# Kernel optimization log

Measured on AMD Instinct MI355X. Metric: run time of the kernel, lower is better.

## Reference

```python
import jax, jax.numpy as jnp
import numpy as np

BT, N = 4, 2048
FIN, FOUT = 512, 128          # GGE in/out; FOUT == PPI output (GAGA constraint)
PIN, POUT = 256, 128          # PPIGE in/out
HEAD = 4
K = POUT // HEAD              # per-head dim = 32
NEG_SLOPE = 0.2
MASK_VAL = -1e30


def setup_inputs() -> dict:
    key = jax.random.key(0)
    ks = jax.random.split(key, 24)
    s = 0.05
    inp = {}
    inp["a"] = jax.random.normal(ks[0], (BT, FIN), jnp.float32)
    inp["bio_a"] = jax.random.normal(ks[1], (BT, N, PIN), jnp.float32)
    inp["A"] = jax.random.randint(ks[2], (BT, N, N), 0, 2, jnp.int32)
    inp["b"] = jax.random.normal(ks[3], (BT, FIN), jnp.float32)
    inp["bio_b"] = jax.random.normal(ks[4], (BT, N, PIN), jnp.float32)
    inp["B"] = jax.random.randint(ks[5], (BT, N, N), 0, 2, jnp.int32)
    # PPIGE_GAT params (shared across both graph branches)
    inp["initW"] = jax.random.normal(ks[6], (POUT, PIN), jnp.float32) * s
    inp["initb"] = jnp.zeros((POUT,), jnp.float32)
    inp["projW"] = jax.random.normal(ks[7], (POUT, POUT), jnp.float32) * s  # no bias
    inp["attw"] = jax.random.normal(ks[8], (HEAD, 2 * K), jnp.float32) * s  # per-head [2k]->1
    inp["attb"] = jnp.zeros((HEAD,), jnp.float32)
    # GGE params
    inp["ggeW1"] = jax.random.normal(ks[9], (128, FIN), jnp.float32) * s
    inp["ggeb1"] = jnp.zeros((128,), jnp.float32)
    inp["ggeW2"] = jax.random.normal(ks[10], (FOUT, 128), jnp.float32) * s
    inp["ggeb2"] = jnp.zeros((FOUT,), jnp.float32)
    # LED params (hidden = FOUT)
    inp["convW"] = jax.random.normal(ks[11], (2 * FOUT, 2 * FOUT), jnp.float32) * s  # k=1 conv
    inp["convb"] = jnp.zeros((2 * FOUT,), jnp.float32)
    inp["ledW1"] = jax.random.normal(ks[12], (FOUT, 4 * FOUT), jnp.float32) * s
    inp["ledb1"] = jnp.zeros((FOUT,), jnp.float32)
    inp["ledW2"] = jax.random.normal(ks[13], (2, FOUT), jnp.float32) * s
    inp["ledb2"] = jnp.zeros((2,), jnp.float32)
    return inp


def _gat_layer(x, adj_mask, projW, attw, attb):
    # x: [B,N,POUT]; adj_mask: [B,N,N] bool
    Bt, n, _ = x.shape
    xh = (x @ projW.T).reshape(Bt, n, HEAD, K).transpose(0, 2, 1, 3)  # [B,h,N,k]
    # score(i,j) = leaky_relu(w1.x_i + w2.x_j + b)  (equivalent to Linear on concat)
    s1 = jnp.einsum('bhnk,hk->bhn', xh, attw[:, :K])
    s2 = jnp.einsum('bhnk,hk->bhn', xh, attw[:, K:])
    scores = jax.nn.leaky_relu(
        s1[..., :, None] + s2[..., None, :] + attb[None, :, None, None], NEG_SLOPE)
    scores = jnp.where(adj_mask[:, None], scores, MASK_VAL)
    att = jax.nn.softmax(scores, axis=-1)                     # [B,h,N,N]
    out = jax.nn.relu(att @ xh)                               # [B,h,N,k]
    return out.transpose(0, 2, 1, 3).reshape(Bt, n, HEAD * K)


def _ppige(bio, adj, initW, initb, projW, attw, attb):
    x = bio @ initW.T + initb
    return _gat_layer(x, adj > 0, projW, attw, attb) + x      # residual; dropout=eval


def _gge(a, W1, b1, W2, b2):
    h = jax.nn.relu(a @ W1.T + b1)
    return jax.nn.relu(h @ W2.T + b2)


def _gaga(G, h):
    # G: [B,N,D], h: [B,D]
    att = jax.nn.softmax(jnp.einsum('bnd,bd->bn', G, h), axis=-1)
    return jnp.einsum('bnd,bn->bd', G, att)


def _led(ea, eb, convW, convb, W1, b1, W2, b2):
    # pointwise conv over the length-2 stack [ea, eb], then maxpool over length
    cnn = jnp.maximum(ea @ convW.T + convb, eb @ convW.T + convb)  # [B,2D]
    x = jax.nn.relu(jnp.concatenate([cnn, ea - eb], axis=1) @ W1.T + b1)
    return x @ W2.T + b2


def reference(a, bio_a, A, b, bio_b, B,
              initW, initb, projW, attw, attb,
              ggeW1, ggeb1, ggeW2, ggeb2,
              convW, convb, ledW1, ledb1, ledW2, ledb2):
    G_a = _ppige(bio_a, A, initW, initb, projW, attw, attb)
    G_b = _ppige(bio_b, B, initW, initb, projW, attw, attb)
    h_a = _gge(a, ggeW1, ggeb1, ggeW2, ggeb2)
    h_b = _gge(b, ggeW1, ggeb1, ggeW2, ggeb2)
    e_a = jnp.concatenate([h_a, _gaga(G_a, h_a)], axis=-1)
    e_b = jnp.concatenate([h_b, _gaga(G_b, h_b)], axis=-1)
    logits = _led(e_a, e_b, convW, convb, ledW1, ledb1, ledW2, ledb2)
    return jax.nn.log_softmax(logits, axis=-1)
```

## Files before the change

kernel.cpp:

```cpp
#include <hip/hip_runtime.h>
#include <hip/hip_bf16.h>
#include <math.h>

#define NN 2048
#define NEG 0.2f
#define LOG2E 1.44269504f

typedef short bf16x8 __attribute__((ext_vector_type(8)));
typedef float f32x16 __attribute__((ext_vector_type(16)));

__device__ __forceinline__ float dot4(float4 a, float4 b) {
  return a.x * b.x + a.y * b.y + a.z * b.z + a.w * b.w;
}

__device__ __forceinline__ unsigned short bfbits(float f) {
  union { __hip_bfloat16 b; unsigned short u; } c;
  c.b = __float2bfloat16(f);
  return c.u;
}

__global__ __launch_bounds__(256) void k12_fused(const float* __restrict__ bioA,
                                                 const float* __restrict__ bioB,
                                                 const float* __restrict__ initW,
                                                 const float* __restrict__ initb,
                                                 const float* __restrict__ projW,
                                                 const float* __restrict__ attw,
                                                 float* __restrict__ xout,
                                                 unsigned short* __restrict__ xhT2,
                                                 float* __restrict__ s1,
                                                 float* __restrict__ s2) {
  __shared__ float As[32][36];
  __shared__ float Ws[32][132];
  __shared__ float xT[128][36];
  const int t = threadIdx.x;
  const int m0 = blockIdx.x * 32;
  const float* A = (m0 < 8192) ? bioA : bioB;
  const int arow0 = (m0 < 8192) ? m0 : (m0 - 8192);
  const int og = t & 31, ig = t >> 5;

  float acc[4][4] = {};
  for (int kt = 0; kt < 256; kt += 32) {
    __syncthreads();
    {
      const int r = t >> 3, kq = t & 7;
      const float4 v = *(const float4*)&A[(arow0 + r) * 256 + kt + kq * 4];
      As[kq * 4 + 0][r] = v.x; As[kq * 4 + 1][r] = v.y;
      As[kq * 4 + 2][r] = v.z; As[kq * 4 + 3][r] = v.w;
    }
#pragma unroll
    for (int u = 0; u < 4; ++u) {
      const int f = u * 256 + t;
      const int o = f >> 3, kq = f & 7;
      const float4 v = *(const float4*)&initW[o * 256 + kt + kq * 4];
      Ws[kq * 4 + 0][o] = v.x; Ws[kq * 4 + 1][o] = v.y;
      Ws[kq * 4 + 2][o] = v.z; Ws[kq * 4 + 3][o] = v.w;
    }
    __syncthreads();
#pragma unroll
    for (int kk = 0; kk < 32; ++kk) {
      const float4 a4 = *(const float4*)&As[kk][ig * 4];
      const float4 w4 = *(const float4*)&Ws[kk][og * 4];
      const float av[4] = {a4.x, a4.y, a4.z, a4.w};
      const float wv[4] = {w4.x, w4.y, w4.z, w4.w};
#pragma unroll
      for (int ii = 0; ii < 4; ++ii)
#pragma unroll
        for (int jj = 0; jj < 4; ++jj) acc[ii][jj] += av[ii] * wv[jj];
    }
  }
  {
    const float4 b4 = *(const float4*)&initb[og * 4];
    const float bj[4] = {b4.x, b4.y, b4.z, b4.w};
#pragma unroll
    for (int ii = 0; ii < 4; ++ii) {
      const int row = m0 + ig * 4 + ii;
      float4 o4;
      o4.x = acc[ii][0] + bj[0]; o4.y = acc[ii][1] + bj[1];
      o4.z = acc[ii][2] + bj[2]; o4.w = acc[ii][3] + bj[3];
      *(float4*)&xout[row * 128 + og * 4] = o4;
    }
#pragma unroll
    for (int jj = 0; jj < 4; ++jj) {
      float4 v;
      v.x = acc[0][jj] + bj[jj]; v.y = acc[1][jj] + bj[jj];
      v.z = acc[2][jj] + bj[jj]; v.w = acc[3][jj] + bj[jj];
      *(float4*)&xT[og * 4 + jj][ig * 4] = v;
    }
  }
  __syncthreads();

  float acc2[4][4] = {};
  for (int kt = 0; kt < 128; kt += 32) {
    __syncthreads();
#pragma unroll
    for (int u = 0; u < 4; ++u) {
      const int f = u * 256 + t;
      const int o = f >> 3, kq = f & 7;
      const float4 v = *(const float4*)&projW[o * 128 + kt + kq * 4];
      Ws[kq * 4 + 0][o] = v.x; Ws[kq * 4 + 1][o] = v.y;
      Ws[kq * 4 + 2][o] = v.z; Ws[kq * 4 + 3][o] = v.w;
    }
    __syncthreads();
#pragma unroll
    for (int kk = 0; kk < 32; ++kk) {
      const float4 a4 = *(const float4*)&xT[kt + kk][ig * 4];
      const float4 w4 = *(const float4*)&Ws[kk][og * 4];
      const float av[4] = {a4.x, a4.y, a4.z, a4.w};
      const float wv[4] = {w4.x, w4.y, w4.z, w4.w};
#pragma unroll
      for (int ii = 0; ii < 4; ++ii)
#pragma unroll
        for (int jj = 0; jj < 4; ++jj) acc2[ii][jj] += av[ii] * wv[jj];
    }
  }
  const int h = og >> 3;
  const int k4i = (og & 7) * 4;
  const int g = m0 >> 13;
  const int bb = (m0 >> 11) & 3;
  const int gb = g * 4 + bb;
  const int n0 = (m0 & 2047) + ig * 4;
  const float4 w1 = *(const float4*)&attw[h * 64 + k4i];
  const float4 w2 = *(const float4*)&attw[h * 64 + 32 + k4i];
  float p1[4], p2[4];
#pragma unroll
  for (int ii = 0; ii < 4; ++ii) {
    float4 v;
    v.x = acc2[ii][0]; v.y = acc2[ii][1]; v.z = acc2[ii][2]; v.w = acc2[ii][3];
    p1[ii] = dot4(v, w1);
    p2[ii] = dot4(v, w2);
  }
  {
    const int mtile = n0 >> 4, jslot = (n0 >> 3) & 1, j8 = n0 & 7;
    const int base2 = ((((gb * 4 + h) * 128 + mtile) * 2 + jslot) * 32) * 8 + j8;
#pragma unroll
    for (int jj = 0; jj < 4; ++jj) {
      const int kin = k4i + jj;
      ushort4 u;
      u.x = bfbits(acc2[0][jj]); u.y = bfbits(acc2[1][jj]);
      u.z = bfbits(acc2[2][jj]); u.w = bfbits(acc2[3][jj]);
      *(ushort4*)&xhT2[base2 + kin * 8] = u;
    }
  }
#pragma unroll
  for (int s = 1; s < 8; s <<= 1) {
#pragma unroll
    for (int ii = 0; ii < 4; ++ii) {
      p1[ii] += __shfl_xor(p1[ii], s);
      p2[ii] += __shfl_xor(p2[ii], s);
    }
  }
  if ((og & 7) == 0) {
#pragma unroll
    for (int ii = 0; ii < 4; ++ii) {
      s1[(gb * 4 + h) * NN + n0 + ii] = p1[ii];
      s2[(gb * 4 + h) * NN + n0 + ii] = p2[ii];
    }
  }
}

#define K3_PROLOGUE                                                           \
  {                                                                           \
    const float* s2g = s2w + gb * 4 * NN;                                     \
    _Pragma("unroll")                                                         \
    for (int u = 0; u < 4; ++u) {                                             \
      const int idx = u * 2048 + t * 4;                                       \
      float4 v = *(const float4*)&s2g[idx];                                   \
      v.x *= LOG2E; v.y *= LOG2E; v.z *= LOG2E; v.w *= LOG2E;                 \
      *(float4*)&s2L[idx] = v;                                                \
    }                                                                         \
  }                                                                           \
  _Pragma("unroll")                                                           \
  for (int r4 = 0; r4 < 4; ++r4) {                                            \
    const int r = wave * 4 + r4;                                              \
    const int* arow = adj + r * NN;                                           \
    int av[32];                                                               \
    _Pragma("unroll")                                                         \
    for (int w = 0; w < 32; ++w) av[w] = __builtin_nontemporal_load(&arow[w * 64 + lane]); \
    _Pragma("unroll")                                                         \
    for (int w = 0; w < 32; ++w) {                                            \
      const unsigned long long mm = __ballot(av[w] > 0);                      \
      if (lane < 2) adjL[r * 66 + 2 * w + lane] = (unsigned int)(mm >> (32 * lane)); \
    }                                                                         \
  }

#define K3_SCORE_BODY(MM)                                                     \
    const int j0 = jlo + 16 * (MM) + jslot * 8;                               \
    const unsigned int wbits = adjL[i * 66 + ((jlo + 16 * (MM)) >> 5)];       \
    const unsigned int bits8 = wbits >> ((((MM) & 1) * 16) + jslot * 8);      \
    const float4 s2a = *(const float4*)&s2L[h * 2048 + j0];                   \
    const float4 s2b = *(const float4*)&s2L[h * 2048 + j0 + 4];               \
    const float sv[8] = {s2a.x, s2a.y, s2a.z, s2a.w,                          \
                         s2b.x, s2b.y, s2b.z, s2b.w};                         \
    union { bf16x8 v; unsigned short u[8]; } af;                              \
    float dsum = 0.f;                                                         \
    _Pragma("unroll")                                                         \
    for (int e = 0; e < 8; ++e) {                                             \
      float s = sc1v + sv[e];                                                 \
      s = fmaxf(s, NEG * s);                                                  \
      float pe = __builtin_amdgcn_exp2f(s);                                   \
      pe = ((bits8 >> e) & 1u) ? pe : 0.f;                                    \
      af.u[e] = bfbits(pe);                                                   \
      dsum += pe;                                                             \
    }                                                                         \
    den += dsum;

__global__ __launch_bounds__(512) void k3_attn(const unsigned short* __restrict__ xhT2,
                                               const float* __restrict__ s1w,
                                               const float* __restrict__ s2w,
                                               const int* __restrict__ adjA,
                                               const int* __restrict__ adjB,
                                               const float* __restrict__ attb,
                                               const float* __restrict__ x,
                                               float* __restrict__ G) {
  __shared__ __align__(16) unsigned char smem3[42240];
  unsigned int* adjL = (unsigned int*)smem3;
  float* s2L = (float*)(smem3 + 8448);
  float* denR = (float*)(smem3 + 41216);
  float* accR = (float*)smem3;

  const int t = threadIdx.x;
  const int wave = t >> 6, lane = t & 63;
  const int p = (int)blockIdx.x;
  const int blk = (p & 7) * 64 + (p >> 3);
  const int g = blk >> 8, b = (blk >> 6) & 3;
  const int i0 = (blk & 63) * 32;
  const int gb = g * 4 + b;
  const int* adj = (g ? adjB : adjA) + (b * NN + i0) * NN;
  K3_PROLOGUE
  __syncthreads();

  const int h = wave & 3;
  const int jhalf = wave >> 2;
  const int jlo = jhalf * 1024;
  const int i = lane & 31;
  const int jslot = lane >> 5;
  const float sc1v = (s1w[(gb * 4 + h) * NN + i0 + i] + attb[h]) * LOG2E;
  const unsigned short* bbase = xhT2 + (gb * 4 + h) * 65536 + jhalf * 32768 + lane * 8;
  f32x16 acc = {0.f, 0.f, 0.f, 0.f, 0.f, 0.f, 0.f, 0.f,
                0.f, 0.f, 0.f, 0.f, 0.f, 0.f, 0.f, 0.f};
  float den = 0.f;

#define K3_CSTEP(RB, MM)                                                      \
  {                                                                           \
    K3_SCORE_BODY(MM)                                                         \
    acc = __builtin_amdgcn_mfma_f32_32x32x16_bf16(af.v, RB, acc, 0, 0, 0);    \
  }

  bf16x8 fa0 = *(const bf16x8*)&bbase[0 * 512];
  bf16x8 fa1 = *(const bf16x8*)&bbase[1 * 512];
  bf16x8 fa2 = *(const bf16x8*)&bbase[2 * 512];
  bf16x8 fa3 = *(const bf16x8*)&bbase[3 * 512];
  bf16x8 fb0 = *(const bf16x8*)&bbase[4 * 512];
  bf16x8 fb1 = *(const bf16x8*)&bbase[5 * 512];
  bf16x8 fb2 = *(const bf16x8*)&bbase[6 * 512];
  bf16x8 fb3 = *(const bf16x8*)&bbase[7 * 512];
  bf16x8 fc0 = *(const bf16x8*)&bbase[8 * 512];
  bf16x8 fc1 = *(const bf16x8*)&bbase[9 * 512];
  bf16x8 fc2 = *(const bf16x8*)&bbase[10 * 512];
  bf16x8 fc3 = *(const bf16x8*)&bbase[11 * 512];
  bf16x8 fd0 = *(const bf16x8*)&bbase[12 * 512];
  bf16x8 fd1 = *(const bf16x8*)&bbase[13 * 512];
  bf16x8 fd2 = *(const bf16x8*)&bbase[14 * 512];
  bf16x8 fd3 = *(const bf16x8*)&bbase[15 * 512];
  __builtin_amdgcn_sched_barrier(0);
  for (int mb = 0; mb < 64; mb += 16) {
    K3_CSTEP(fa0, mb + 0)
    K3_CSTEP(fa1, mb + 1)
    K3_CSTEP(fa2, mb + 2)
    K3_CSTEP(fa3, mb + 3)
    __builtin_amdgcn_sched_barrier(0);
    if (mb < 48) {
      fa0 = *(const bf16x8*)&bbase[(mb + 16) * 512];
      fa1 = *(const bf16x8*)&bbase[(mb + 17) * 512];
      fa2 = *(const bf16x8*)&bbase[(mb + 18) * 512];
      fa3 = *(const bf16x8*)&bbase[(mb + 19) * 512];
    }
    __builtin_amdgcn_sched_barrier(0);
    K3_CSTEP(fb0, mb + 4)
    K3_CSTEP(fb1, mb + 5)
    K3_CSTEP(fb2, mb + 6)
    K3_CSTEP(fb3, mb + 7)
    __builtin_amdgcn_sched_barrier(0);
    if (mb < 48) {
      fb0 = *(const bf16x8*)&bbase[(mb + 20) * 512];
      fb1 = *(const bf16x8*)&bbase[(mb + 21) * 512];
      fb2 = *(const bf16x8*)&bbase[(mb + 22) * 512];
      fb3 = *(const bf16x8*)&bbase[(mb + 23) * 512];
    }
    __builtin_amdgcn_sched_barrier(0);
    K3_CSTEP(fc0, mb + 8)
    K3_CSTEP(fc1, mb + 9)
    K3_CSTEP(fc2, mb + 10)
    K3_CSTEP(fc3, mb + 11)
    __builtin_amdgcn_sched_barrier(0);
    if (mb < 48) {
      fc0 = *(const bf16x8*)&bbase[(mb + 24) * 512];
      fc1 = *(const bf16x8*)&bbase[(mb + 25) * 512];
      fc2 = *(const bf16x8*)&bbase[(mb + 26) * 512];
      fc3 = *(const bf16x8*)&bbase[(mb + 27) * 512];
    }
    __builtin_amdgcn_sched_barrier(0);
    K3_CSTEP(fd0, mb + 12)
    K3_CSTEP(fd1, mb + 13)
    K3_CSTEP(fd2, mb + 14)
    K3_CSTEP(fd3, mb + 15)
    __builtin_amdgcn_sched_barrier(0);
    if (mb < 48) {
      fd0 = *(const bf16x8*)&bbase[(mb + 28) * 512];
      fd1 = *(const bf16x8*)&bbase[(mb + 29) * 512];
      fd2 = *(const bf16x8*)&bbase[(mb + 30) * 512];
      fd3 = *(const bf16x8*)&bbase[(mb + 31) * 512];
    }
    __builtin_amdgcn_sched_barrier(0);
  }
#undef K3_CSTEP

  den += __shfl_xor(den, 32);
  if (lane < 32) denR[(h * 2 + jhalf) * 32 + lane] = den;
  __syncthreads();
  if (jhalf == 1) {
#pragma unroll
    for (int r = 0; r < 16; ++r) accR[(h * 16 + r) * 65 + lane] = acc[r];
  }
  __syncthreads();
  if (jhalf == 0) {
#pragma unroll
    for (int r = 0; r < 16; ++r) {
      const int row = (r & 3) + 8 * (r >> 2) + 4 * jslot;
      const float dinv = 1.f / (denR[(h * 2 + 0) * 32 + row] + denR[(h * 2 + 1) * 32 + row]);
      const int off = (gb * NN + i0 + row) * 128 + h * 32 + i;
      const float av2 = acc[r] + accR[(h * 16 + r) * 65 + lane];
      G[off] = fmaxf(av2 * dinv, 0.f) + x[off];
    }
  }
}

__global__ __launch_bounds__(256) void k4h_gge(const float* __restrict__ a_in,
                                               const float* __restrict__ b_in,
                                               const float* __restrict__ ggeW1,
                                               const float* __restrict__ ggeb1,
                                               const float* __restrict__ ggeW2,
                                               const float* __restrict__ ggeb2,
                                               float* __restrict__ hvbuf,
                                               float* __restrict__ e) {
  __shared__ float inL[512];
  __shared__ float h1L[128];
  const int t = threadIdx.x;
  const int wave = t >> 6, lane = t & 63;
  const int g = blockIdx.x >> 2, b = blockIdx.x & 3;
  const int gb2 = g * 4 + b;
  const float* inp = (g ? b_in : a_in) + b * 512;
  if (t < 128) *(float4*)&inL[t * 4] = *(const float4*)&inp[t * 4];
  __syncthreads();
  for (int p = 0; p < 16; ++p) {
    const int o0 = p * 8 + wave * 2;
    const float* w0 = &ggeW1[o0 * 512 + lane * 8];
    const float* w1 = &ggeW1[(o0 + 1) * 512 + lane * 8];
    const float4 i0v = *(const float4*)&inL[lane * 8];
    const float4 i1v = *(const float4*)&inL[lane * 8 + 4];
    float s0 = dot4(*(const float4*)&w0[0], i0v) + dot4(*(const float4*)&w0[4], i1v);
    float s1v = dot4(*(const float4*)&w1[0], i0v) + dot4(*(const float4*)&w1[4], i1v);
#pragma unroll
    for (int s = 1; s < 64; s <<= 1) { s0 += __shfl_xor(s0, s); s1v += __shfl_xor(s1v, s); }
    if (lane == 0) {
      h1L[o0] = fmaxf(s0 + ggeb1[o0], 0.f);
      h1L[o0 + 1] = fmaxf(s1v + ggeb1[o0 + 1], 0.f);
    }
  }
  __syncthreads();
  for (int p = 0; p < 16; ++p) {
    const int o0 = p * 8 + wave * 2;
    const float2 w0 = *(const float2*)&ggeW2[o0 * 128 + lane * 2];
    const float2 w1 = *(const float2*)&ggeW2[(o0 + 1) * 128 + lane * 2];
    const float2 hvv = *(const float2*)&h1L[lane * 2];
    float s0 = w0.x * hvv.x + w0.y * hvv.y;
    float s1v = w1.x * hvv.x + w1.y * hvv.y;
#pragma unroll
    for (int s = 1; s < 64; s <<= 1) { s0 += __shfl_xor(s0, s); s1v += __shfl_xor(s1v, s); }
    if (lane == 0) {
      const float v0 = fmaxf(s0 + ggeb2[o0], 0.f);
      const float v1 = fmaxf(s1v + ggeb2[o0 + 1], 0.f);
      hvbuf[gb2 * 128 + o0] = v0;
      hvbuf[gb2 * 128 + o0 + 1] = v1;
      e[gb2 * 256 + o0] = v0;
      e[gb2 * 256 + o0 + 1] = v1;
    }
  }
}

__global__ __launch_bounds__(256) void k4a_gaga(const float* __restrict__ G,
                                                const float* __restrict__ hv,
                                                float* __restrict__ wsumC,
                                                float* __restrict__ mzC) {
  __shared__ float lgL[128];
  __shared__ float pL[128];
  __shared__ float red[256];
  __shared__ float red2[2][128];
  const int t = threadIdx.x;
  const int wave = t >> 6, lane = t & 63;
  const int gb = blockIdx.x >> 4, chunk = blockIdx.x & 15;
  const float2 hvv = *(const float2*)&hv[gb * 128 + lane * 2];
  const float* Gb = G + (gb * NN + chunk * 128) * 128;
  const int nbase = wave * 32;
  for (int q = 0; q < 32; ++q) {
    const int n = nbase + q;
    const float2 gv = *(const float2*)&Gb[n * 128 + lane * 2];
    float part = gv.x * hvv.x + gv.y * hvv.y;
#pragma unroll
    for (int s = 1; s < 64; s <<= 1) part += __shfl_xor(part, s);
    if (lane == 0) lgL[n] = part;
  }
  __syncthreads();
  red[t] = (t < 128) ? lgL[t] : -1e30f;
  __syncthreads();
#pragma unroll
  for (int s = 128; s > 0; s >>= 1) {
    if (t < s) red[t] = fmaxf(red[t], red[t + s]);
    __syncthreads();
  }
  const float mc = red[0];
  __syncthreads();
  if (t < 128) {
    const float pv = __expf(lgL[t] - mc);
    pL[t] = pv;
    red[t] = pv;
  } else red[t] = 0.f;
  __syncthreads();
#pragma unroll
  for (int s = 128; s > 0; s >>= 1) {
    if (t < s) red[t] += red[t + s];
    __syncthreads();
  }
  const float zc = red[0];
  __syncthreads();
  const int d = t & 127, half = t >> 7;
  const float* Gh = Gb + (half * 64) * 128;
  float acc = 0.f;
  for (int q = 0; q < 64; ++q) acc += pL[half * 64 + q] * Gh[q * 128 + d];
  red2[half][d] = acc;
  __syncthreads();
  if (t < 128) wsumC[(gb * 16 + chunk) * 128 + t] = red2[0][t] + red2[1][t];
  if (t == 0) {
    mzC[(gb * 16 + chunk) * 2 + 0] = mc;
    mzC[(gb * 16 + chunk) * 2 + 1] = zc;
  }
}

__global__ __launch_bounds__(256) void k5_led(const float* __restrict__ e,
                                              const float* __restrict__ wsumC,
                                              const float* __restrict__ mzC,
                                              const float* __restrict__ convW,
                                              const float* __restrict__ convb,
                                              const float* __restrict__ ledW1,
                                              const float* __restrict__ ledb1,
                                              const float* __restrict__ ledW2,
                                              const float* __restrict__ ledb2,
                                              float* __restrict__ out) {
  __shared__ float eaL[256], ebL[256], uL[512], xL[128], lgL[2];
  const int t = threadIdx.x;
  const int wave = t >> 6, lane = t & 63;
  const int bt = blockIdx.x;
  const int gba = bt, gbb = 4 + bt;
  if (t < 128) {
    eaL[t] = e[gba * 256 + t];
    ebL[t] = e[gbb * 256 + t];
    float ma = -1e30f, mb2 = -1e30f;
#pragma unroll
    for (int c = 0; c < 16; ++c) {
      ma = fmaxf(ma, mzC[(gba * 16 + c) * 2]);
      mb2 = fmaxf(mb2, mzC[(gbb * 16 + c) * 2]);
    }
    float Za = 0.f, Zb = 0.f, sa = 0.f, sb = 0.f;
#pragma unroll
    for (int c = 0; c < 16; ++c) {
      const float wa = __expf(mzC[(gba * 16 + c) * 2] - ma);
      const float wb = __expf(mzC[(gbb * 16 + c) * 2] - mb2);
      Za += mzC[(gba * 16 + c) * 2 + 1] * wa;
      Zb += mzC[(gbb * 16 + c) * 2 + 1] * wb;
      sa += wsumC[(gba * 16 + c) * 128 + t] * wa;
      sb += wsumC[(gbb * 16 + c) * 128 + t] * wb;
    }
    eaL[128 + t] = sa / Za;
    ebL[128 + t] = sb / Zb;
  }
  __syncthreads();
  uL[256 + t] = eaL[t] - ebL[t];
  const float4 ea4 = *(const float4*)&eaL[lane * 4];
  const float4 eb4 = *(const float4*)&ebL[lane * 4];
  for (int p = 0; p < 32; ++p) {
    const int o0 = p * 8 + wave * 2;
    const float4 w0 = *(const float4*)&convW[o0 * 256 + lane * 4];
    const float4 w1 = *(const float4*)&convW[(o0 + 1) * 256 + lane * 4];
    float sa0 = dot4(w0, ea4), sb0 = dot4(w0, eb4);
    float sa1 = dot4(w1, ea4), sb1 = dot4(w1, eb4);
#pragma unroll
    for (int s = 1; s < 64; s <<= 1) {
      sa0 += __shfl_xor(sa0, s); sb0 += __shfl_xor(sb0, s);
      sa1 += __shfl_xor(sa1, s); sb1 += __shfl_xor(sb1, s);
    }
    if (lane == 0) {
      const float c0 = convb[o0], c1 = convb[o0 + 1];
      uL[o0] = fmaxf(sa0 + c0, sb0 + c0);
      uL[o0 + 1] = fmaxf(sa1 + c1, sb1 + c1);
    }
  }
  __syncthreads();
  for (int p = 0; p < 16; ++p) {
    const int o0 = p * 8 + wave * 2;
    const float* w0 = &ledW1[o0 * 512 + lane * 8];
    const float* w1 = &ledW1[(o0 + 1) * 512 + lane * 8];
    const float4 u0 = *(const float4*)&uL[lane * 8];
    const float4 u1 = *(const float4*)&uL[lane * 8 + 4];
    float s0 = dot4(*(const float4*)&w0[0], u0) + dot4(*(const float4*)&w0[4], u1);
    float s1v = dot4(*(const float4*)&w1[0], u0) + dot4(*(const float4*)&w1[4], u1);
#pragma unroll
    for (int s = 1; s < 64; s <<= 1) { s0 += __shfl_xor(s0, s); s1v += __shfl_xor(s1v, s); }
    if (lane == 0) {
      xL[o0] = fmaxf(s0 + ledb1[o0], 0.f);
      xL[o0 + 1] = fmaxf(s1v + ledb1[o0 + 1], 0.f);
    }
  }
  __syncthreads();
  if (wave < 2) {
    const float2 w = *(const float2*)&ledW2[wave * 128 + lane * 2];
    const float2 xv = *(const float2*)&xL[lane * 2];
    float s0 = w.x * xv.x + w.y * xv.y;
#pragma unroll
    for (int s = 1; s < 64; s <<= 1) s0 += __shfl_xor(s0, s);
    if (lane == 0) lgL[wave] = s0 + ledb2[wave];
  }
  __syncthreads();
  if (t == 0) {
    const float l0 = lgL[0], l1 = lgL[1];
    const float m = fmaxf(l0, l1);
    const float za = __expf(l0 - m) + __expf(l1 - m);
    const float lz = __logf(za);
    out[bt * 2 + 0] = l0 - m - lz;
    out[bt * 2 + 1] = l1 - m - lz;
  }
}

extern "C" void kernel_launch(void* const* d_in, const int* in_sizes, int n_in,
                              void* d_out, int out_size, void* d_ws, size_t ws_size,
                              hipStream_t stream) {
  (void)in_sizes; (void)n_in; (void)out_size; (void)ws_size;
  const float* a     = (const float*)d_in[0];
  const float* bioA  = (const float*)d_in[1];
  const int*   A     = (const int*)d_in[2];
  const float* b     = (const float*)d_in[3];
  const float* bioB  = (const float*)d_in[4];
  const int*   B     = (const int*)d_in[5];
  const float* initW = (const float*)d_in[6];
  const float* initb = (const float*)d_in[7];
  const float* projW = (const float*)d_in[8];
  const float* attw  = (const float*)d_in[9];
  const float* attb  = (const float*)d_in[10];
  const float* ggeW1 = (const float*)d_in[11];
  const float* ggeb1 = (const float*)d_in[12];
  const float* ggeW2 = (const float*)d_in[13];
  const float* ggeb2 = (const float*)d_in[14];
  const float* convW = (const float*)d_in[15];
  const float* convb = (const float*)d_in[16];
  const float* ledW1 = (const float*)d_in[17];
  const float* ledb1 = (const float*)d_in[18];
  const float* ledW2 = (const float*)d_in[19];
  const float* ledb2 = (const float*)d_in[20];

  float* ws = (float*)d_ws;
  float*          x     = ws;
  unsigned short* xhT2  = (unsigned short*)(ws + 2097152);
  float*          s1    = ws + 3145728;
  float*          s2    = ws + 3211264;
  float*          G     = ws + 3276800;
  float*          mzC   = ws + 5373952;
  float*          wsumC = ws + 5390336;
  float*          hv    = ws + 5406736;
  float*          e     = ws + 5407760;
  float* out = (float*)d_out;

  k12_fused<<<512, 256, 0, stream>>>(bioA, bioB, initW, initb, projW, attw,
                                     x, xhT2, s1, s2);
  k3_attn<<<512, 512, 0, stream>>>(xhT2, s1, s2, A, B, attb, x, G);
  k4h_gge<<<8, 256, 0, stream>>>(a, b, ggeW1, ggeb1, ggeW2, ggeb2, hv, e);
  k4a_gaga<<<128, 256, 0, stream>>>(G, hv, wsumC, mzC);
  k5_led<<<4, 256, 0, stream>>>(e, wsumC, mzC, convW, convb, ledW1, ledb1,
                                ledW2, ledb2, out);
}
```

Measured before the change: 182.4 us.

## Fuse GGE into projection kernel and GAGA partial softmax into attention epilogue

The GGE MLP now runs on eight extra blocks appended to the projection kernel launch. The GAGA logits, per-chunk softmax max and sum, and the weighted sum over G are computed in the attention kernel epilogue, one chunk per 32-row tile. This removes two kernel launches and the separate re-read of G by the old GAGA kernel. In exchange the final LED kernel must merge 64 chunks per graph instead of 16, and the epilogue re-reads G from global memory just after writing it.

Measured after the change: 165.0 us (median of 2 runs). 1.11x faster.

```diff
diff --git a/kernel.cpp b/kernel.cpp
--- a/kernel.cpp
+++ b/kernel.cpp
@@ -25,14 +25,70 @@
                                                  const float* __restrict__ initb,
                                                  const float* __restrict__ projW,
                                                  const float* __restrict__ attw,
+                                                 const float* __restrict__ a_in,
+                                                 const float* __restrict__ b_in,
+                                                 const float* __restrict__ ggeW1,
+                                                 const float* __restrict__ ggeb1,
+                                                 const float* __restrict__ ggeW2,
+                                                 const float* __restrict__ ggeb2,
                                                  float* __restrict__ xout,
                                                  unsigned short* __restrict__ xhT2,
                                                  float* __restrict__ s1,
-                                                 float* __restrict__ s2) {
+                                                 float* __restrict__ s2,
+                                                 float* __restrict__ hvbuf,
+                                                 float* __restrict__ e) {
   __shared__ float As[32][36];
   __shared__ float Ws[32][132];
   __shared__ float xT[128][36];
   const int t = threadIdx.x;
+  const int wave = t >> 6, lane = t & 63;
+
+  if (blockIdx.x >= 512) {
+    float* inL = (float*)As;
+    float* h1L = ((float*)As) + 512;
+    const int bb2 = (int)blockIdx.x - 512;
+    const int g = bb2 >> 2, b = bb2 & 3;
+    const int gb2 = g * 4 + b;
+    const float* inp = (g ? b_in : a_in) + b * 512;
+    if (t < 128) *(float4*)&inL[t * 4] = *(const float4*)&inp[t * 4];
+    __syncthreads();
+    for (int p = 0; p < 16; ++p) {
+      const int o0 = p * 8 + wave * 2;
+      const float* w0 = &ggeW1[o0 * 512 + lane * 8];
+      const float* w1 = &ggeW1[(o0 + 1) * 512 + lane * 8];
+      const float4 i0v = *(const float4*)&inL[lane * 8];
+      const float4 i1v = *(const float4*)&inL[lane * 8 + 4];
+      float s0 = dot4(*(const float4*)&w0[0], i0v) + dot4(*(const float4*)&w0[4], i1v);
+      float s1v = dot4(*(const float4*)&w1[0], i0v) + dot4(*(const float4*)&w1[4], i1v);
+#pragma unroll
+      for (int s = 1; s < 64; s <<= 1) { s0 += __shfl_xor(s0, s); s1v += __shfl_xor(s1v, s); }
+      if (lane == 0) {
+        h1L[o0] = fmaxf(s0 + ggeb1[o0], 0.f);
+        h1L[o0 + 1] = fmaxf(s1v + ggeb1[o0 + 1], 0.f);
+      }
+    }
+    __syncthreads();
+    for (int p = 0; p < 16; ++p) {
+      const int o0 = p * 8 + wave * 2;
+      const float2 w0 = *(const float2*)&ggeW2[o0 * 128 + lane * 2];
+      const float2 w1 = *(const float2*)&ggeW2[(o0 + 1) * 128 + lane * 2];
+      const float2 hvv = *(const float2*)&h1L[lane * 2];
+      float s0 = w0.x * hvv.x + w0.y * hvv.y;
+      float s1v = w1.x * hvv.x + w1.y * hvv.y;
+#pragma unroll
+      for (int s = 1; s < 64; s <<= 1) { s0 += __shfl_xor(s0, s); s1v += __shfl_xor(s1v, s); }
+      if (lane == 0) {
+        const float v0 = fmaxf(s0 + ggeb2[o0], 0.f);
+        const float v1 = fmaxf(s1v + ggeb2[o0 + 1], 0.f);
+        hvbuf[gb2 * 128 + o0] = v0;
+        hvbuf[gb2 * 128 + o0 + 1] = v1;
+        e[gb2 * 256 + o0] = v0;
+        e[gb2 * 256 + o0 + 1] = v1;
+      }
+    }
+    return;
+  }
+
   const int m0 = blockIdx.x * 32;
   const float* A = (m0 < 8192) ? bioA : bioB;
   const int arow0 = (m0 < 8192) ? m0 : (m0 - 8192);
@@ -211,12 +267,17 @@
                                                const int* __restrict__ adjB,
                                                const float* __restrict__ attb,
                                                const float* __restrict__ x,
-                                               float* __restrict__ G) {
+                                               const float* __restrict__ hv,
+                                               float* __restrict__ G,
+                                               float* __restrict__ wsumC,
+                                               float* __restrict__ mzC) {
   __shared__ __align__(16) unsigned char smem3[42240];
   unsigned int* adjL = (unsigned int*)smem3;
   float* s2L = (float*)(smem3 + 8448);
   float* denR = (float*)(smem3 + 41216);
   float* accR = (float*)smem3;
+  float* lgW = (float*)(smem3 + 16640);
+  float* pL = (float*)(smem3 + 17280);
 
   const int t = threadIdx.x;
   const int wave = t >> 6, lane = t & 63;
@@ -225,6 +286,7 @@
   const int g = blk >> 8, b = (blk >> 6) & 3;
   const int i0 = (blk & 63) * 32;
   const int gb = g * 4 + b;
+  const int cidx = gb * 64 + (blk & 63);
   const int* adj = (g ? adjB : adjA) + (b * NN + i0) * NN;
   K3_PROLOGUE
   __syncthreads();
@@ -323,6 +385,7 @@
     for (int r = 0; r < 16; ++r) accR[(h * 16 + r) * 65 + lane] = acc[r];
   }
   __syncthreads();
+  const float hvv = hv[gb * 128 + h * 32 + i];
   if (jhalf == 0) {
 #pragma unroll
     for (int r = 0; r < 16; ++r) {
@@ -330,119 +393,39 @@
       const float dinv = 1.f / (denR[(h * 2 + 0) * 32 + row] + denR[(h * 2 + 1) * 32 + row]);
       const int off = (gb * NN + i0 + row) * 128 + h * 32 + i;
       const float av2 = acc[r] + accR[(h * 16 + r) * 65 + lane];
-      G[off] = fmaxf(av2 * dinv, 0.f) + x[off];
-    }
-  }
-}
-
-__global__ __launch_bounds__(256) void k4h_gge(const float* __restrict__ a_in,
-                                               const float* __restrict__ b_in,
-                                               const float* __restrict__ ggeW1,
-                                               const float* __restrict__ ggeb1,
-                                               const float* __restrict__ ggeW2,
-                                               const float* __restrict__ ggeb2,
-                                               float* __restrict__ hvbuf,
-                                               float* __restrict__ e) {
-  __shared__ float inL[512];
-  __shared__ float h1L[128];
-  const int t = threadIdx.x;
-  const int wave = t >> 6, lane = t & 63;
-  const int g = blockIdx.x >> 2, b = blockIdx.x & 3;
-  const int gb2 = g * 4 + b;
-  const float* inp = (g ? b_in : a_in) + b * 512;
-  if (t < 128) *(float4*)&inL[t * 4] = *(const float4*)&inp[t * 4];
-  __syncthreads();
-  for (int p = 0; p < 16; ++p) {
-    const int o0 = p * 8 + wave * 2;
-    const float* w0 = &ggeW1[o0 * 512 + lane * 8];
-    const float* w1 = &ggeW1[(o0 + 1) * 512 + lane * 8];
-    const float4 i0v = *(const float4*)&inL[lane * 8];
-    const float4 i1v = *(const float4*)&inL[lane * 8 + 4];
-    float s0 = dot4(*(const float4*)&w0[0], i0v) + dot4(*(const float4*)&w0[4], i1v);
-    float s1v = dot4(*(const float4*)&w1[0], i0v) + dot4(*(const float4*)&w1[4], i1v);
-#pragma unroll
-    for (int s = 1; s < 64; s <<= 1) { s0 += __shfl_xor(s0, s); s1v += __shfl_xor(s1v, s); }
-    if (lane == 0) {
-      h1L[o0] = fmaxf(s0 + ggeb1[o0], 0.f);
-      h1L[o0 + 1] = fmaxf(s1v + ggeb1[o0 + 1], 0.f);
-    }
-  }
-  __syncthreads();
-  for (int p = 0; p < 16; ++p) {
-    const int o0 = p * 8 + wave * 2;
-    const float2 w0 = *(const float2*)&ggeW2[o0 * 128 + lane * 2];
-    const float2 w1 = *(const float2*)&ggeW2[(o0 + 1) * 128 + lane * 2];
-    const float2 hvv = *(const float2*)&h1L[lane * 2];
-    float s0 = w0.x * hvv.x + w0.y * hvv.y;
-    float s1v = w1.x * hvv.x + w1.y * hvv.y;
-#pragma unroll
-    for (int s = 1; s < 64; s <<= 1) { s0 += __shfl_xor(s0, s); s1v += __shfl_xor(s1v, s); }
-    if (lane == 0) {
-      const float v0 = fmaxf(s0 + ggeb2[o0], 0.f);
-      const float v1 = fmaxf(s1v + ggeb2[o0 + 1], 0.f);
-      hvbuf[gb2 * 128 + o0] = v0;
-      hvbuf[gb2 * 128 + o0 + 1] = v1;
-      e[gb2 * 256 + o0] = v0;
-      e[gb2 * 256 + o0 + 1] = v1;
-    }
-  }
-}
-
-__global__ __launch_bounds__(256) void k4a_gaga(const float* __restrict__ G,
-                                                const float* __restrict__ hv,
-                                                float* __restrict__ wsumC,
-                                                float* __restrict__ mzC) {
-  __shared__ float lgL[128];
-  __shared__ float pL[128];
-  __shared__ float red[256];
-  __shared__ float red2[2][128];
-  const int t = threadIdx.x;
-  const int wave = t >> 6, lane = t & 63;
-  const int gb = blockIdx.x >> 4, chunk = blockIdx.x & 15;
-  const float2 hvv = *(const float2*)&hv[gb * 128 + lane * 2];
-  const float* Gb = G + (gb * NN + chunk * 128) * 128;
-  const int nbase = wave * 32;
-  for (int q = 0; q < 32; ++q) {
-    const int n = nbase + q;
-    const float2 gv = *(const float2*)&Gb[n * 128 + lane * 2];
-    float part = gv.x * hvv.x + gv.y * hvv.y;
-#pragma unroll
-    for (int s = 1; s < 64; s <<= 1) part += __shfl_xor(part, s);
-    if (lane == 0) lgL[n] = part;
-  }
-  __syncthreads();
-  red[t] = (t < 128) ? lgL[t] : -1e30f;
-  __syncthreads();
-#pragma unroll
-  for (int s = 128; s > 0; s >>= 1) {
-    if (t < s) red[t] = fmaxf(red[t], red[t + s]);
-    __syncthreads();
-  }
-  const float mc = red[0];
-  __syncthreads();
-  if (t < 128) {
-    const float pv = __expf(lgL[t] - mc);
+      const float gval = fmaxf(av2 * dinv, 0.f) + x[off];
+      G[off] = gval;
+      float c = gval * hvv;
+      c += __shfl_xor(c, 1); c += __shfl_xor(c, 2); c += __shfl_xor(c, 4);
+      c += __shfl_xor(c, 8); c += __shfl_xor(c, 16);
+      if (i == 0) lgW[h * 32 + row] = c;
+    }
+  }
+  __syncthreads();
+  if (t < 32) {
+    float lg = lgW[t] + lgW[32 + t] + lgW[64 + t] + lgW[96 + t];
+    float m = lg;
+    m = fmaxf(m, __shfl_xor(m, 1)); m = fmaxf(m, __shfl_xor(m, 2));
+    m = fmaxf(m, __shfl_xor(m, 4)); m = fmaxf(m, __shfl_xor(m, 8));
+    m = fmaxf(m, __shfl_xor(m, 16));
+    const float pv = __expf(lg - m);
+    float z = pv;
+    z += __shfl_xor(z, 1); z += __shfl_xor(z, 2); z += __shfl_xor(z, 4);
+    z += __shfl_xor(z, 8); z += __shfl_xor(z, 16);
     pL[t] = pv;
-    red[t] = pv;
-  } else red[t] = 0.f;
-  __syncthreads();
-#pragma unroll
-  for (int s = 128; s > 0; s >>= 1) {
-    if (t < s) red[t] += red[t + s];
-    __syncthreads();
-  }
-  const float zc = red[0];
-  __syncthreads();
-  const int d = t & 127, half = t >> 7;
-  const float* Gh = Gb + (half * 64) * 128;
-  float acc = 0.f;
-  for (int q = 0; q < 64; ++q) acc += pL[half * 64 + q] * Gh[q * 128 + d];
-  red2[half][d] = acc;
-  __syncthreads();
-  if (t < 128) wsumC[(gb * 16 + chunk) * 128 + t] = red2[0][t] + red2[1][t];
-  if (t == 0) {
-    mzC[(gb * 16 + chunk) * 2 + 0] = mc;
-    mzC[(gb * 16 + chunk) * 2 + 1] = zc;
+    if (t == 0) { mzC[cidx * 2] = m; mzC[cidx * 2 + 1] = z; }
+  }
+  __syncthreads();
+  if (jhalf == 0) {
+    float wp = 0.f;
+#pragma unroll
+    for (int r = 0; r < 16; ++r) {
+      const int row = (r & 3) + 8 * (r >> 2) + 4 * jslot;
+      const int off = (gb * NN + i0 + row) * 128 + h * 32 + i;
+      wp += pL[row] * G[off];
+    }
+    wp += __shfl_xor(wp, 32);
+    if (jslot == 0) wsumC[cidx * 128 + h * 32 + i] = wp;
   }
 }
 
@@ -465,20 +448,18 @@
     eaL[t] = e[gba * 256 + t];
     ebL[t] = e[gbb * 256 + t];
     float ma = -1e30f, mb2 = -1e30f;
-#pragma unroll
-    for (int c = 0; c < 16; ++c) {
-      ma = fmaxf(ma, mzC[(gba * 16 + c) * 2]);
-      mb2 = fmaxf(mb2, mzC[(gbb * 16 + c) * 2]);
+    for (int c = 0; c < 64; ++c) {
+      ma = fmaxf(ma, mzC[(gba * 64 + c) * 2]);
+      mb2 = fmaxf(mb2, mzC[(gbb * 64 + c) * 2]);
     }
     float Za = 0.f, Zb = 0.f, sa = 0.f, sb = 0.f;
-#pragma unroll
-    for (int c = 0; c < 16; ++c) {
-      const float wa = __expf(mzC[(gba * 16 + c) * 2] - ma);
-      const float wb = __expf(mzC[(gbb * 16 + c) * 2] - mb2);
-      Za += mzC[(gba * 16 + c) * 2 + 1] * wa;
-      Zb += mzC[(gbb * 16 + c) * 2 + 1] * wb;
-      sa += wsumC[(gba * 16 + c) * 128 + t] * wa;
-      sb += wsumC[(gbb * 16 + c) * 128 + t] * wb;
+    for (int c = 0; c < 64; ++c) {
+      const float wa = __expf(mzC[(gba * 64 + c) * 2] - ma);
+      const float wb = __expf(mzC[(gbb * 64 + c) * 2] - mb2);
+      Za += mzC[(gba * 64 + c) * 2 + 1] * wa;
+      Zb += mzC[(gbb * 64 + c) * 2 + 1] * wb;
+      sa += wsumC[(gba * 64 + c) * 128 + t] * wa;
+      sb += wsumC[(gbb * 64 + c) * 128 + t] * wb;
     }
     eaL[128 + t] = sa / Za;
     ebL[128 + t] = sb / Zb;
@@ -573,16 +554,16 @@
   float*          s2    = ws + 3211264;
   float*          G     = ws + 3276800;
   float*          mzC   = ws + 5373952;
-  float*          wsumC = ws + 5390336;
-  float*          hv    = ws + 5406736;
-  float*          e     = ws + 5407760;
+  float*          wsumC = ws + 5374976;
+  float*          hv    = ws + 5440512;
+  float*          e     = ws + 5441536;
   float* out = (float*)d_out;
 
-  k12_fused<<<512, 256, 0, stream>>>(bioA, bioB, initW, initb, projW, attw,
-                                     x, xhT2, s1, s2);
-  k3_attn<<<512, 512, 0, stream>>>(xhT2, s1, s2, A, B, attb, x, G);
-  k4h_gge<<<8, 256, 0, stream>>>(a, b, ggeW1, ggeb1, ggeW2, ggeb2, hv, e);
-  k4a_gaga<<<128, 256, 0, stream>>>(G, hv, wsumC, mzC);
+  k12_fused<<<520, 256, 0, stream>>>(bioA, bioB, initW, initb, projW, attw,
+                                     a, b, ggeW1, ggeb1, ggeW2, ggeb2,
+                                     x, xhT2, s1, s2, hv, e);
+  k3_attn<<<512, 512, 0, stream>>>(xhT2, s1, s2, A, B, attb, x, hv, G,
+                                   wsumC, mzC);
   k5_led<<<4, 256, 0, stream>>>(e, wsumC, mzC, convW, convb, ledW1, ledb1,
                                 ledW2, ledb2, out);
 }
```
